# Performance work log

Hardware: AMD Instinct MI355X
Metric: run time of the kernel (lower is better)

Reference implementation:

```python
import jax, jax.numpy as jnp
import numpy as np

NUM_HEADS = 16
HEAD_DIM = 64
NEG_INF = -1000000000.0


def rotary_embedding(x, seq_len, head_dim):
    # x: (batch, seq, heads, head_dim)
    positions = jnp.arange(seq_len)
    dim_pairs = jnp.arange(0, head_dim, 2)
    freqs = 1.0 / 10000.0 ** (dim_pairs / head_dim)
    angles = positions[:, None] * freqs[None, :]          # (seq, head_dim/2)
    cos = jnp.cos(angles)[:, None, :]                     # (seq, 1, head_dim/2) -> broadcast over heads
    sin = jnp.sin(angles)[:, None, :]
    x1 = x[..., ::2]
    x2 = x[..., 1::2]
    out1 = x1 * cos - x2 * sin
    out2 = x1 * sin + x2 * cos
    return jnp.stack([out1, out2], axis=-1).reshape(x.shape)


def setup_inputs() -> dict:
    key = jax.random.key(0)
    k1, k2, k3 = jax.random.split(key, 3)
    batch, seq_len, embed_dim = 2, 2048, 1024
    x = jax.random.normal(k1, (batch, seq_len, embed_dim), dtype=jnp.float32)
    W_qkv = jax.random.normal(k2, (embed_dim, 3 * NUM_HEADS * HEAD_DIM), dtype=jnp.float32) * 0.02
    W_out = jax.random.normal(k3, (NUM_HEADS * HEAD_DIM, embed_dim), dtype=jnp.float32) * 0.02
    return {"x": x, "W_qkv": W_qkv, "W_out": W_out}


def reference(x, W_qkv, W_out):
    batch, seq_len, embed_dim = x.shape
    qkv = jnp.einsum('bse,ef->bsf', x, W_qkv)
    qkv = qkv.reshape(batch, seq_len, 3, NUM_HEADS, HEAD_DIM)
    q, k, v = qkv[:, :, 0], qkv[:, :, 1], qkv[:, :, 2]
    q = rotary_embedding(q, seq_len, HEAD_DIM)
    k = rotary_embedding(k, seq_len, HEAD_DIM)
    scale = 1.0 / jnp.sqrt(jnp.asarray(HEAD_DIM, dtype=x.dtype))
    scores = jnp.einsum('bqhd,bkhd->bhqk', q, k) * scale   # (B,H,S,S)
    mask = jnp.tril(jnp.ones((seq_len, seq_len), dtype=bool))[None, None, :, :]
    scores = jnp.where(mask, scores, NEG_INF)
    weights = jax.nn.softmax(scores, axis=-1)
    out = jnp.einsum('bhqk,bkhd->bqhd', weights, v)
    out = out.reshape(batch, seq_len, NUM_HEADS * HEAD_DIM)
    return jnp.einsum('bsf,fe->bse', out, W_out)
```

## Files before the change

### kernel.cpp

```cpp
#include <hip/hip_runtime.h>
#include <hip/hip_bf16.h>

typedef __attribute__((ext_vector_type(8))) short short8;
typedef __attribute__((ext_vector_type(4))) float float4v;

__global__ __launch_bounds__(256) void prep_all(
    const float* __restrict__ x, __hip_bfloat16* __restrict__ xb,
    float2* __restrict__ tab,
    const float* __restrict__ Wqkv, const float* __restrict__ Wout,
    __hip_bfloat16* __restrict__ WqkvT, __hip_bfloat16* __restrict__ WoutT) {
  __shared__ __hip_bfloat16 tile[32][33];
  const int id = blockIdx.x;
  if (id < 4096) {
    const int i = id * 256 + threadIdx.x;
    const float4 v = *(const float4*)(x + (size_t)i * 4);
    __hip_bfloat16 o[4];
    o[0] = __float2bfloat16(v.x); o[1] = __float2bfloat16(v.y);
    o[2] = __float2bfloat16(v.z); o[3] = __float2bfloat16(v.w);
    *(uint2*)(xb + (size_t)i * 4) = *(const uint2*)o;
    return;
  }
  if (id < 4352) {
    const int i = (id - 4096) * 256 + threadIdx.x;
    const int s = i >> 5, p = i & 31;
    const float freq = powf(10000.f, -(float)(p * 2) / 64.f);
    float sn, cs;
    sincosf((float)s * freq, &sn, &cs);
    tab[i] = make_float2(cs, sn);
    return;
  }
  const float* in;
  __hip_bfloat16* out;
  int C, bx, by;
  if (id < 7424) {
    const int lid = id - 4352;
    in = Wqkv; out = WqkvT; C = 3072; bx = lid % 96; by = lid / 96;
  } else {
    const int lid = id - 7424;
    in = Wout; out = WoutT; C = 1024; bx = lid & 31; by = lid >> 5;
  }
  const int R = 1024;
  const int c0 = bx * 32, r0 = by * 32;
  const int tx = threadIdx.x & 31, ty = threadIdx.x >> 5;
  #pragma unroll
  for (int i = ty; i < 32; i += 8)
    tile[i][tx] = __float2bfloat16(in[(size_t)(r0 + i) * C + (c0 + tx)]);
  __syncthreads();
  #pragma unroll
  for (int i = ty; i < 32; i += 8)
    out[(size_t)(c0 + i) * R + (r0 + tx)] = tile[tx][i];
}

template <typename OutT, int BM, int BN>
__global__ __launch_bounds__(256) void gemm_bt(
    const __hip_bfloat16* __restrict__ A,
    const __hip_bfloat16* __restrict__ Bt,
    OutT* __restrict__ C,
    int M, int N, int K) {
  __shared__ __hip_bfloat16 lA[BM][64];
  __shared__ __hip_bfloat16 lB[BN][64];
  constexpr int NI = BM / 32, NJ = BN / 32;
  const int t = threadIdx.x;
  const int lane = t & 63, wave = t >> 6;
  const int quad = lane >> 4, ln = lane & 15;
  const int m0 = blockIdx.y * BM, n0 = blockIdx.x * BN;
  const int wm = (wave >> 1) * (BM / 2), wn = (wave & 1) * (BN / 2);
  const int srow = lane >> 3;
  const int schunk = ((lane & 7) ^ srow) * 8;

  float4v acc[NI][NJ];
  #pragma unroll
  for (int i = 0; i < NI; ++i)
    #pragma unroll
    for (int j = 0; j < NJ; ++j)
      acc[i][j] = (float4v){0.f, 0.f, 0.f, 0.f};

  for (int kt = 0; kt < K; kt += 64) {
    __syncthreads();
    #pragma unroll
    for (int g = 0; g < BM / 32; ++g) {
      const int rbase = wave * (BM / 4) + g * 8;
      __builtin_amdgcn_global_load_lds(
          (const __attribute__((address_space(1))) void*)
              (A + (size_t)(m0 + rbase + srow) * K + kt + schunk),
          (__attribute__((address_space(3))) void*)&lA[rbase][0], 16, 0, 0);
    }
    #pragma unroll
    for (int g = 0; g < BN / 32; ++g) {
      const int rbase = wave * (BN / 4) + g * 8;
      __builtin_amdgcn_global_load_lds(
          (const __attribute__((address_space(1))) void*)
              (Bt + (size_t)(n0 + rbase + srow) * K + kt + schunk),
          (__attribute__((address_space(3))) void*)&lB[rbase][0], 16, 0, 0);
    }
    __syncthreads();
    #pragma unroll
    for (int step = 0; step < 2; ++step) {
      short8 af[NI], bf[NJ];
      #pragma unroll
      for (int i = 0; i < NI; ++i)
        af[i] = *(const short8*)&lA[wm + i * 16 + ln][((step * 4 + quad) ^ (ln & 7)) * 8];
      #pragma unroll
      for (int j = 0; j < NJ; ++j)
        bf[j] = *(const short8*)&lB[wn + j * 16 + ln][((step * 4 + quad) ^ (ln & 7)) * 8];
      #pragma unroll
      for (int i = 0; i < NI; ++i)
        #pragma unroll
        for (int j = 0; j < NJ; ++j)
          acc[i][j] = __builtin_amdgcn_mfma_f32_16x16x32_bf16(af[i], bf[j], acc[i][j], 0, 0, 0);
    }
  }
  #pragma unroll
  for (int i = 0; i < NI; ++i)
    #pragma unroll
    for (int j = 0; j < NJ; ++j)
      #pragma unroll
      for (int r = 0; r < 4; ++r) {
        const int row = m0 + wm + i * 16 + quad * 4 + r;
        const int col = n0 + wn + j * 16 + ln;
        if constexpr (__is_same(OutT, float))
          C[(size_t)row * N + col] = acc[i][j][r];
        else
          C[(size_t)row * N + col] = __float2bfloat16(acc[i][j][r]);
      }
}

__global__ __launch_bounds__(256) void qkv_prep(
    const __hip_bfloat16* __restrict__ qkv,
    const float2* __restrict__ tab,
    __hip_bfloat16* __restrict__ Q,
    __hip_bfloat16* __restrict__ K,
    __hip_bfloat16* __restrict__ Vt) {
  __shared__ __hip_bfloat16 tile[64][65];
  const int s0 = blockIdx.x * 64;
  const int bh = blockIdx.y;
  const int h = bh & 15, b = bh >> 4;
  const int t = threadIdx.x;

  const int pr = t & 31, sl = t >> 5;
  const int d0 = pr * 2;
  const float qs = 0.125f * 1.44269504088896340736f;
  #pragma unroll
  for (int ss = sl; ss < 64; ss += 8) {
    const int s = s0 + ss;
    const float2 cssn = tab[(size_t)s * 32 + pr];
    const float cs = cssn.x, sn = cssn.y;
    const size_t in_base = (size_t)(b * 2048 + s) * 3072;
    const size_t o = ((size_t)bh * 2048 + s) * 64 + d0;

    __hip_bfloat162 q2 = *(const __hip_bfloat162*)&qkv[in_base + h * 64 + d0];
    float x1 = __bfloat162float(q2.x), x2 = __bfloat162float(q2.y);
    __hip_bfloat162 qo;
    qo.x = __float2bfloat16((x1 * cs - x2 * sn) * qs);
    qo.y = __float2bfloat16((x1 * sn + x2 * cs) * qs);
    *(__hip_bfloat162*)&Q[o] = qo;

    __hip_bfloat162 k2 = *(const __hip_bfloat162*)&qkv[in_base + 1024 + h * 64 + d0];
    x1 = __bfloat162float(k2.x); x2 = __bfloat162float(k2.y);
    __hip_bfloat162 ko;
    ko.x = __float2bfloat16(x1 * cs - x2 * sn);
    ko.y = __float2bfloat16(x1 * sn + x2 * cs);
    *(__hip_bfloat162*)&K[o] = ko;
  }

  const int tx = t & 63, ty = t >> 6;
  #pragma unroll
  for (int i = ty; i < 64; i += 4)
    tile[i][tx] = qkv[(size_t)(b * 2048 + s0 + i) * 3072 + 2048 + h * 64 + tx];
  __syncthreads();
  #pragma unroll
  for (int i = ty; i < 64; i += 4)
    Vt[((size_t)bh * 64 + i) * 2048 + s0 + tx] = tile[tx][i];
}

__global__ __launch_bounds__(256) void attention(
    const __hip_bfloat16* __restrict__ Q,
    const __hip_bfloat16* __restrict__ K,
    const __hip_bfloat16* __restrict__ Vt,
    __hip_bfloat16* __restrict__ attn) {
  __shared__ __hip_bfloat16 lK[2][64][64];
  __shared__ __hip_bfloat16 lV[2][64][64];
  __shared__ __hip_bfloat16 lO[4][16][64];
  const int t = threadIdx.x;
  const int lane = t & 63, w = t >> 6;
  const int quad = lane >> 4, ln = lane & 15;
  const int id = blockIdx.x;
  const int bh = id & 31;
  const int j = id >> 5;
  const int k2 = j >> 3, g = j & 7;
  const int qt = 8 * k2 + ((k2 & 1) ? (7 - g) : g);
  const int q0 = qt * 64;
  const size_t base = (size_t)bh * 2048 * 64;
  const __hip_bfloat16* Qb = Q + base;
  const __hip_bfloat16* Kb = K + base;
  const __hip_bfloat16* Vb = Vt + base;
  const int b = bh >> 4, h = bh & 15;

  const int srow = lane >> 3;
  const int schunkV = ((lane & 7) ^ srow) * 8;
  const int rb0 = w * 16;
  const int sig_base = (ln >> 2) * 8 + (ln & 3);

  #pragma unroll
  for (int g2 = 0; g2 < 2; ++g2) {
    const int rbase = rb0 + g2 * 8;
    const int schunkK = (((lane & 7) ^ srow) ^ (g2 << 2)) * 8;
    __builtin_amdgcn_global_load_lds(
        (const __attribute__((address_space(1))) void*)
            (Kb + (size_t)(rbase + srow) * 64 + schunkK),
        (__attribute__((address_space(3))) void*)&lK[0][rbase][0], 16, 0, 0);
    __builtin_amdgcn_global_load_lds(
        (const __attribute__((address_space(1))) void*)
            (Vb + (size_t)(rbase + srow) * 2048 + schunkV),
        (__attribute__((address_space(3))) void*)&lV[0][rbase][0], 16, 0, 0);
  }

  short8 qf[2];
  {
    const size_t qrow = (size_t)(q0 + w * 16 + ln) * 64;
    qf[0] = *(const short8*)(Qb + qrow + quad * 8);
    qf[1] = *(const short8*)(Qb + qrow + 32 + quad * 8);
  }

  float4v acc_o[4];
  #pragma unroll
  for (int dt = 0; dt < 4; ++dt) acc_o[dt] = (float4v){0.f, 0.f, 0.f, 0.f};
  float suml = 0.f;

  for (int kt = 0; kt <= qt; ++kt) {
    const int buf = kt & 1;
    __syncthreads();

    if (kt < qt) {
      #pragma unroll
      for (int g2 = 0; g2 < 2; ++g2) {
        const int rbase = rb0 + g2 * 8;
        const int schunkK = (((lane & 7) ^ srow) ^ (g2 << 2)) * 8;
        __builtin_amdgcn_global_load_lds(
            (const __attribute__((address_space(1))) void*)
                (Kb + (size_t)((kt + 1) * 64 + rbase + srow) * 64 + schunkK),
            (__attribute__((address_space(3))) void*)&lK[buf ^ 1][rbase][0], 16, 0, 0);
        __builtin_amdgcn_global_load_lds(
            (const __attribute__((address_space(1))) void*)
                (Vb + (size_t)(rbase + srow) * 2048 + (kt + 1) * 64 + schunkV),
            (__attribute__((address_space(3))) void*)&lV[buf ^ 1][rbase][0], 16, 0, 0);
      }
    }

    float4v s4[4];
    #pragma unroll
    for (int nt = 0; nt < 4; ++nt) {
      const int krow = sig_base + ((nt & 1) << 2) + ((nt >> 1) << 5);
      const int k7 = (krow & 7) ^ (((krow >> 3) & 1) << 2);
      float4v a = (float4v){0.f, 0.f, 0.f, 0.f};
      #pragma unroll
      for (int step = 0; step < 2; ++step) {
        short8 kf = *(const short8*)&lK[buf][krow][((step * 4 + quad) ^ k7) * 8];
        a = __builtin_amdgcn_mfma_f32_16x16x32_bf16(kf, qf[step], a, 0, 0, 0);
      }
      s4[nt] = a;
    }
    if (kt == qt) {
      const int qr = q0 + w * 16 + ln;
      #pragma unroll
      for (int nt = 0; nt < 4; ++nt)
        #pragma unroll
        for (int r = 0; r < 4; ++r) {
          const int kglob = kt * 64 + quad * 8 + ((nt & 1) << 2) + r + ((nt >> 1) << 5);
          if (kglob > qr) s4[nt][r] = -64.f;
        }
    }
    #pragma unroll
    for (int nt = 0; nt < 4; ++nt)
      #pragma unroll
      for (int r = 0; r < 4; ++r) {
        s4[nt][r] = __builtin_amdgcn_exp2f(s4[nt][r]);
        suml += s4[nt][r];
      }
    #pragma unroll
    for (int s = 0; s < 2; ++s) {
      union { short8 v; short e[8]; } pb;
      #pragma unroll
      for (int i = 0; i < 4; ++i) {
        __hip_bfloat16 b0 = __float2bfloat16(s4[2 * s][i]);
        __hip_bfloat16 b1 = __float2bfloat16(s4[2 * s + 1][i]);
        pb.e[i] = *reinterpret_cast<short*>(&b0);
        pb.e[4 + i] = *reinterpret_cast<short*>(&b1);
      }
      #pragma unroll
      for (int dt = 0; dt < 4; ++dt) {
        short8 vf = *(const short8*)&lV[buf][dt * 16 + ln][((s * 4 + quad) ^ (ln & 7)) * 8];
        acc_o[dt] = __builtin_amdgcn_mfma_f32_16x16x32_bf16(vf, pb.v, acc_o[dt], 0, 0, 0);
      }
    }
  }

  float l0 = suml + __shfl_xor(suml, 16);
  const float inv = 1.0f / (l0 + __shfl_xor(l0, 32));

  #pragma unroll
  for (int dt = 0; dt < 4; ++dt) {
    union { uint2 u; short e[4]; } pk;
    #pragma unroll
    for (int r = 0; r < 4; ++r) {
      __hip_bfloat16 bv = __float2bfloat16(acc_o[dt][r] * inv);
      pk.e[r] = *reinterpret_cast<short*>(&bv);
    }
    *(uint2*)&lO[w][ln][dt * 16 + quad * 4] = pk.u;
  }

  const int orow = lane >> 2;
  const int od = (lane & 3) * 16;
  const uint4 w0 = *(const uint4*)&lO[w][orow][od];
  const uint4 w1 = *(const uint4*)&lO[w][orow][od + 8];
  const size_t rg = (size_t)(b * 2048 + q0 + w * 16 + orow);
  *(uint4*)&attn[rg * 1024 + h * 64 + od] = w0;
  *(uint4*)&attn[rg * 1024 + h * 64 + od + 8] = w1;
}

extern "C" void kernel_launch(void* const* d_in, const int* in_sizes, int n_in,
                              void* d_out, int out_size, void* d_ws, size_t ws_size,
                              hipStream_t stream) {
  const float* x    = (const float*)d_in[0];
  const float* Wqkv = (const float*)d_in[1];
  const float* Wout = (const float*)d_in[2];
  float* out = (float*)d_out;

  __hip_bfloat16* ws = (__hip_bfloat16*)d_ws;
  __hip_bfloat16* xb    = ws;
  __hip_bfloat16* WqkvT = xb    + (size_t)4096 * 1024;
  __hip_bfloat16* WoutT = WqkvT + (size_t)3072 * 1024;
  __hip_bfloat16* qkv   = WoutT + (size_t)1024 * 1024;
  __hip_bfloat16* Q     = qkv   + (size_t)4096 * 3072;
  __hip_bfloat16* K     = Q     + (size_t)32 * 2048 * 64;
  __hip_bfloat16* Vt    = K     + (size_t)32 * 2048 * 64;
  __hip_bfloat16* attn  = Vt    + (size_t)32 * 2048 * 64;
  float2*         tab   = (float2*)(attn + (size_t)4096 * 1024);

  prep_all<<<8448, 256, 0, stream>>>(x, xb, tab, Wqkv, Wout, WqkvT, WoutT);
  gemm_bt<__hip_bfloat16, 128, 128><<<dim3(3072 / 128, 4096 / 128), 256, 0, stream>>>(xb, WqkvT, qkv, 4096, 3072, 1024);
  qkv_prep<<<dim3(32, 32), 256, 0, stream>>>(qkv, tab, Q, K, Vt);
  attention<<<1024, 256, 0, stream>>>(Q, K, Vt, attn);
  gemm_bt<float, 128, 64><<<dim3(1024 / 64, 4096 / 128), 256, 0, stream>>>(attn, WoutT, out, 4096, 1024, 1024);
}
```

Baseline: 172.1 us.

## Fuse Q rotary into attention and vectorize transpose/rope stores

Q rotary embedding and scaling now happen inside the attention kernel, which reads raw qkv rows and the cos/sin table directly, so the intermediate Q buffer is never written or re-read. The qkv_prep kernel handles only K rope, using 16-byte vector loads and stores, and the V transpose, which now uses wider packed LDS reads and global writes. The weight transpose in prep_all also packs two bf16 values per store. The trade-off is extra loads and arithmetic at the start of each attention block, plus strided qkv reads for Q.

Measured after the change: 172.4 us (median of 2 runs). No clear change (+0.1%).

```diff
diff --git a/kernel.cpp b/kernel.cpp
--- a/kernel.cpp
+++ b/kernel.cpp
@@ -3,6 +3,24 @@
 
 typedef __attribute__((ext_vector_type(8))) short short8;
 typedef __attribute__((ext_vector_type(4))) float float4v;
+
+__device__ inline short8 rope8(short8 raw, float4 tA, float4 tB, float scale) {
+  float c[4] = {tA.x, tA.z, tB.x, tB.z};
+  float s[4] = {tA.y, tA.w, tB.y, tB.w};
+  union { short8 v; short e[8]; } in, out;
+  in.v = raw;
+  #pragma unroll
+  for (int j = 0; j < 4; ++j) {
+    __hip_bfloat16 h1 = *reinterpret_cast<__hip_bfloat16*>(&in.e[2 * j]);
+    __hip_bfloat16 h2 = *reinterpret_cast<__hip_bfloat16*>(&in.e[2 * j + 1]);
+    const float x1 = __bfloat162float(h1), x2 = __bfloat162float(h2);
+    __hip_bfloat16 o1 = __float2bfloat16((x1 * c[j] - x2 * s[j]) * scale);
+    __hip_bfloat16 o2 = __float2bfloat16((x1 * s[j] + x2 * c[j]) * scale);
+    out.e[2 * j]     = *reinterpret_cast<short*>(&o1);
+    out.e[2 * j + 1] = *reinterpret_cast<short*>(&o2);
+  }
+  return out.v;
+}
 
 __global__ __launch_bounds__(256) void prep_all(
     const float* __restrict__ x, __hip_bfloat16* __restrict__ xb,
@@ -46,9 +64,14 @@
   for (int i = ty; i < 32; i += 8)
     tile[i][tx] = __float2bfloat16(in[(size_t)(r0 + i) * C + (c0 + tx)]);
   __syncthreads();
-  #pragma unroll
-  for (int i = ty; i < 32; i += 8)
-    out[(size_t)(c0 + i) * R + (r0 + tx)] = tile[tx][i];
+  const int sx = threadIdx.x & 15, sy = threadIdx.x >> 4;
+  #pragma unroll
+  for (int i = sy; i < 32; i += 16) {
+    union { unsigned u; short e[2]; } pk;
+    pk.e[0] = *reinterpret_cast<short*>(&tile[2 * sx][i]);
+    pk.e[1] = *reinterpret_cast<short*>(&tile[2 * sx + 1][i]);
+    *(unsigned*)&out[(size_t)(c0 + i) * R + r0 + 2 * sx] = pk.u;
+  }
 }
 
 template <typename OutT, int BM, int BN>
@@ -128,53 +151,47 @@
 __global__ __launch_bounds__(256) void qkv_prep(
     const __hip_bfloat16* __restrict__ qkv,
     const float2* __restrict__ tab,
-    __hip_bfloat16* __restrict__ Q,
     __hip_bfloat16* __restrict__ K,
     __hip_bfloat16* __restrict__ Vt) {
-  __shared__ __hip_bfloat16 tile[64][65];
+  __shared__ __hip_bfloat16 tile[64][68];
   const int s0 = blockIdx.x * 64;
   const int bh = blockIdx.y;
   const int h = bh & 15, b = bh >> 4;
   const int t = threadIdx.x;
 
-  const int pr = t & 31, sl = t >> 5;
-  const int d0 = pr * 2;
-  const float qs = 0.125f * 1.44269504088896340736f;
-  #pragma unroll
-  for (int ss = sl; ss < 64; ss += 8) {
+  const int dd = (t & 7) * 8;
+  const int sl = t >> 3;
+  #pragma unroll
+  for (int ss = sl; ss < 64; ss += 32) {
     const int s = s0 + ss;
-    const float2 cssn = tab[(size_t)s * 32 + pr];
-    const float cs = cssn.x, sn = cssn.y;
-    const size_t in_base = (size_t)(b * 2048 + s) * 3072;
-    const size_t o = ((size_t)bh * 2048 + s) * 64 + d0;
-
-    __hip_bfloat162 q2 = *(const __hip_bfloat162*)&qkv[in_base + h * 64 + d0];
-    float x1 = __bfloat162float(q2.x), x2 = __bfloat162float(q2.y);
-    __hip_bfloat162 qo;
-    qo.x = __float2bfloat16((x1 * cs - x2 * sn) * qs);
-    qo.y = __float2bfloat16((x1 * sn + x2 * cs) * qs);
-    *(__hip_bfloat162*)&Q[o] = qo;
-
-    __hip_bfloat162 k2 = *(const __hip_bfloat162*)&qkv[in_base + 1024 + h * 64 + d0];
-    x1 = __bfloat162float(k2.x); x2 = __bfloat162float(k2.y);
-    __hip_bfloat162 ko;
-    ko.x = __float2bfloat16(x1 * cs - x2 * sn);
-    ko.y = __float2bfloat16(x1 * sn + x2 * cs);
-    *(__hip_bfloat162*)&K[o] = ko;
-  }
-
-  const int tx = t & 63, ty = t >> 6;
-  #pragma unroll
-  for (int i = ty; i < 64; i += 4)
-    tile[i][tx] = qkv[(size_t)(b * 2048 + s0 + i) * 3072 + 2048 + h * 64 + tx];
+    short8 kv = *(const short8*)&qkv[(size_t)(b * 2048 + s) * 3072 + 1024 + h * 64 + dd];
+    const float4 tA = *(const float4*)&tab[(size_t)s * 32 + (dd >> 1)];
+    const float4 tB = *(const float4*)&tab[(size_t)s * 32 + (dd >> 1) + 2];
+    *(short8*)&K[((size_t)bh * 2048 + s) * 64 + dd] = rope8(kv, tA, tB, 1.0f);
+  }
+
+  const int dgrp = (t & 15) * 4;
+  const int srow = t >> 4;
+  #pragma unroll
+  for (int i = srow; i < 64; i += 16) {
+    ushort4 v4 = *(const ushort4*)&qkv[(size_t)(b * 2048 + s0 + i) * 3072 + 2048 + h * 64 + dgrp];
+    *(ushort4*)&tile[i][dgrp] = v4;
+  }
   __syncthreads();
-  #pragma unroll
-  for (int i = ty; i < 64; i += 4)
-    Vt[((size_t)bh * 64 + i) * 2048 + s0 + tx] = tile[tx][i];
+  const int vx = t & 15, vy = t >> 4;
+  #pragma unroll
+  for (int d = vy; d < 64; d += 16) {
+    union { ushort4 v; short e[4]; } pk;
+    #pragma unroll
+    for (int jj = 0; jj < 4; ++jj)
+      pk.e[jj] = *reinterpret_cast<short*>(&tile[4 * vx + jj][d]);
+    *(ushort4*)&Vt[((size_t)bh * 64 + d) * 2048 + s0 + 4 * vx] = pk.v;
+  }
 }
 
 __global__ __launch_bounds__(256) void attention(
-    const __hip_bfloat16* __restrict__ Q,
+    const __hip_bfloat16* __restrict__ qkv,
+    const float2* __restrict__ tab,
     const __hip_bfloat16* __restrict__ K,
     const __hip_bfloat16* __restrict__ Vt,
     __hip_bfloat16* __restrict__ attn) {
@@ -191,7 +208,6 @@
   const int qt = 8 * k2 + ((k2 & 1) ? (7 - g) : g);
   const int q0 = qt * 64;
   const size_t base = (size_t)bh * 2048 * 64;
-  const __hip_bfloat16* Qb = Q + base;
   const __hip_bfloat16* Kb = K + base;
   const __hip_bfloat16* Vb = Vt + base;
   const int b = bh >> 4, h = bh & 15;
@@ -217,9 +233,17 @@
 
   short8 qf[2];
   {
-    const size_t qrow = (size_t)(q0 + w * 16 + ln) * 64;
-    qf[0] = *(const short8*)(Qb + qrow + quad * 8);
-    qf[1] = *(const short8*)(Qb + qrow + 32 + quad * 8);
+    const float qs = 0.125f * 1.44269504088896340736f;
+    const int s = q0 + w * 16 + ln;
+    const size_t qrow = (size_t)(b * 2048 + s) * 3072 + h * 64;
+    short8 raw0 = *(const short8*)&qkv[qrow + quad * 8];
+    short8 raw1 = *(const short8*)&qkv[qrow + 32 + quad * 8];
+    const float4 ta = *(const float4*)&tab[(size_t)s * 32 + quad * 4];
+    const float4 tb = *(const float4*)&tab[(size_t)s * 32 + quad * 4 + 2];
+    const float4 tc = *(const float4*)&tab[(size_t)s * 32 + 16 + quad * 4];
+    const float4 td = *(const float4*)&tab[(size_t)s * 32 + 16 + quad * 4 + 2];
+    qf[0] = rope8(raw0, ta, tb, qs);
+    qf[1] = rope8(raw1, tc, td, qs);
   }
 
   float4v acc_o[4];
@@ -339,7 +363,7 @@
 
   prep_all<<<8448, 256, 0, stream>>>(x, xb, tab, Wqkv, Wout, WqkvT, WoutT);
   gemm_bt<__hip_bfloat16, 128, 128><<<dim3(3072 / 128, 4096 / 128), 256, 0, stream>>>(xb, WqkvT, qkv, 4096, 3072, 1024);
-  qkv_prep<<<dim3(32, 32), 256, 0, stream>>>(qkv, tab, Q, K, Vt);
-  attention<<<1024, 256, 0, stream>>>(Q, K, Vt, attn);
+  qkv_prep<<<dim3(32, 32), 256, 0, stream>>>(qkv, tab, K, Vt);
+  attention<<<1024, 256, 0, stream>>>(qkv, tab, K, Vt, attn);
   gemm_bt<float, 128, 64><<<dim3(1024 / 64, 4096 / 128), 256, 0, stream>>>(attn, WoutT, out, 4096, 1024, 1024);
 }
```
